# Performance work log

Measured on AMD Instinct MI355X. Metric: run time of the kernel, lower is better.

## Reference

```python
import jax, jax.numpy as jnp
import numpy as np

N_ITEM = 100000
DIV_TRADEOFF = 0.1


def setup_inputs() -> dict:
    key = jax.random.key(0)
    ks = jax.random.split(key, 9)
    B, K, L, D_LLM, H = 512, 8, 50, 768, 128
    return {
        "user_id": jax.random.randint(ks[0], (B,), 0, 50000),
        "base_model_preds": jax.random.randint(ks[1], (B, K, L), 0, N_ITEM + 1),
        "preference_in": jax.random.normal(ks[2], (B, H), jnp.float32),
        "pos_label": jax.random.normal(ks[3], (B, K), jnp.float32),
        "neg_label": jax.random.normal(ks[4], (B, K), jnp.float32),
        "user_embeddings": jax.random.normal(ks[5], (50000, H), jnp.float32) * 0.01,
        "item_embeddings": jax.random.normal(ks[6], (N_ITEM + 1, D_LLM), jnp.float32) * 0.02,
        "W_proj": jax.random.normal(ks[7], (D_LLM, H), jnp.float32) * (1.0 / np.sqrt(D_LLM)),
        "b_proj": jax.random.normal(ks[8], (H,), jnp.float32) * 0.01,
    }


def reference(user_id, base_model_preds, preference_in, pos_label, neg_label,
              user_embeddings, item_embeddings, W_proj, b_proj):
    B, K, L = base_model_preds.shape
    # masked gather-embed: ids outside (0, n_item] map to a zero row
    valid = (base_model_preds > 0) & (base_model_preds <= N_ITEM)
    safe_ids = jnp.where(valid, base_model_preds, 0)
    focus_llm = item_embeddings[safe_ids] * valid[..., None].astype(item_embeddings.dtype)  # [B,K,L,D_llm]
    # linear projection to hidden (bias applied everywhere, matching nn.Linear on zeroed rows)
    bm = jnp.einsum('bkld,dh->bklh', focus_llm, W_proj) + b_proj  # [B,K,L,H]
    # time-decay weighted sum over sequence positions
    time_w = 1.0 / jnp.log2(jnp.arange(L, dtype=jnp.float32) + 2.0)  # [L]
    basemodel_emb = jnp.einsum('bklh,l->bkh', bm, time_w)  # [B,K,H]
    # preference = DIEN(...) + user_emb  (DIEN output modeled by preference_in)
    preference = preference_in + user_embeddings[user_id]  # [B,H]
    wgts_org = jnp.einsum('bkh,bh->bk', basemodel_emb, preference)
    wgts = jax.nn.softmax(wgts_org, axis=-1)  # [B,K]
    pos_scores = jnp.sum(pos_label * wgts, axis=1)
    neg_scores = jnp.sum(neg_label * wgts, axis=1)
    loss = -jnp.sum(jax.nn.log_sigmoid(pos_scores - neg_scores))
    # diversity regularizer (use_div=True)
    cov_wgt = jax.lax.stop_gradient(wgts[:, None, :] + wgts[:, :, None])  # [B,K,K]
    cov_mask = 1.0 - jnp.eye(K, dtype=wgts.dtype)  # [K,K]
    gram = jnp.einsum('bih,bjh->bij', basemodel_emb, basemodel_emb) ** 2
    loss_div = DIV_TRADEOFF * jnp.mean(cov_mask[None] * gram * cov_wgt)
    return loss + loss_div
```

## Files before the change

### kernel.cpp

```cpp
#include <hip/hip_runtime.h>
#include <math.h>

#define B_SZ 512
#define K_SZ 8
#define L_SZ 50
#define DLLM 768
#define H_SZ 128
#define N_ITEM 100000
#define DIV_TRADEOFF 0.1f
#define M_PAD 100032

typedef float  f32x4 __attribute__((ext_vector_type(4)));
typedef short  bf16x8 __attribute__((ext_vector_type(8)));
typedef unsigned int u32x4 __attribute__((ext_vector_type(4)));
typedef unsigned short u16x8 __attribute__((ext_vector_type(8)));

__device__ __forceinline__ unsigned short f2bf(float f) {
    unsigned u = __float_as_uint(f);
    u += 0x7fffu + ((u >> 16) & 1u);
    return (unsigned short)(u >> 16);
}

__device__ __forceinline__ void gload_lds16(const void* g, void* l) {
    __builtin_amdgcn_global_load_lds(
        (const __attribute__((address_space(1))) unsigned*)g,
        (__attribute__((address_space(3))) unsigned*)l, 16, 0, 0);
}

__global__ __launch_bounds__(256) void k_wt(
    const float* __restrict__ W,
    unsigned short* __restrict__ Wt,
    float* __restrict__ out)
{
    __shared__ float tile[64][65];
    const int kb = blockIdx.x >> 1;
    const int nb = blockIdx.x & 1;
    const int t  = threadIdx.x;
    if (blockIdx.x == 0 && t == 0) out[0] = 0.0f;

    const int r  = t >> 2;
    const int c0 = (t & 3) * 16;
    #pragma unroll
    for (int j = 0; j < 4; ++j) {
        const float4 v = *(const float4*)(W + (size_t)(kb * 64 + r) * H_SZ + nb * 64 + c0 + j * 4);
        tile[r][c0 + j * 4 + 0] = v.x;
        tile[r][c0 + j * 4 + 1] = v.y;
        tile[r][c0 + j * 4 + 2] = v.z;
        tile[r][c0 + j * 4 + 3] = v.w;
    }
    __syncthreads();
    const int n  = t >> 2;
    const int k0 = (t & 3) * 16;
    u16x8 lo, hi;
    #pragma unroll
    for (int j = 0; j < 8; ++j) lo[j] = f2bf(tile[k0 + j][n]);
    #pragma unroll
    for (int j = 0; j < 8; ++j) hi[j] = f2bf(tile[k0 + 8 + j][n]);
    unsigned short* dst = Wt + (size_t)(nb * 64 + n) * DLLM + kb * 64 + k0;
    *(u16x8*)(dst)     = lo;
    *(u16x8*)(dst + 8) = hi;
}

__global__ __launch_bounds__(256) void k_proj(
    const float* __restrict__ item,
    const unsigned short* __restrict__ Wt,
    unsigned short* __restrict__ projb)
{
    __shared__ unsigned short As[2][64 * 64];
    __shared__ unsigned short Bs[3][128 * 64];

    const int t    = threadIdx.x;
    const int brow = blockIdx.x * 64;
    const int w    = t >> 6;
    const int lane = t & 63;
    const int nl   = lane & 15;
    const int g    = lane >> 4;
    const int key  = nl & 7;
    const int r    = w * 16 + nl;

    const int b_nsub = (lane >> 3);
    const int b_gl   = lane & 7;
    const int b_key  = b_nsub & 7;
    auto STAGE_B = [&](int d, int c) {
        const int kc = c * 64;
        #pragma unroll
        for (int i = 0; i < 4; ++i) {
            const int n_t = w * 32 + i * 8 + b_nsub;
            const int kb  = (b_gl ^ b_key) * 8;
            gload_lds16(Wt + (size_t)n_t * DLLM + kc + kb,
                        &Bs[d][w * 2048 + i * 512]);
        }
    };

    const int ar    = t >> 2;
    const int aseg  = t & 3;
    const int akey  = ar & 7;
    const int arowS = (brow + ar <= N_ITEM) ? (brow + ar) : N_ITEM;
    const float* __restrict__ asrc = item + (size_t)arowS * DLLM + aseg * 16;

    f32x4 La[4];
    auto A_ISSUE = [&](int c) {
        const float* p = asrc + c * 64;
        #pragma unroll
        for (int j = 0; j < 4; ++j) La[j] = *(const f32x4*)(p + j * 4);
    };
    auto A_WRITE = [&](int d) {
        unsigned p0, p1, p2, p3, p4, p5, p6, p7;
        asm("v_cvt_pk_bf16_f32 %0, %1, %2" : "=v"(p0) : "v"(La[0].x), "v"(La[0].y));
        asm("v_cvt_pk_bf16_f32 %0, %1, %2" : "=v"(p1) : "v"(La[0].z), "v"(La[0].w));
        asm("v_cvt_pk_bf16_f32 %0, %1, %2" : "=v"(p2) : "v"(La[1].x), "v"(La[1].y));
        asm("v_cvt_pk_bf16_f32 %0, %1, %2" : "=v"(p3) : "v"(La[1].z), "v"(La[1].w));
        asm("v_cvt_pk_bf16_f32 %0, %1, %2" : "=v"(p4) : "v"(La[2].x), "v"(La[2].y));
        asm("v_cvt_pk_bf16_f32 %0, %1, %2" : "=v"(p5) : "v"(La[2].z), "v"(La[2].w));
        asm("v_cvt_pk_bf16_f32 %0, %1, %2" : "=v"(p6) : "v"(La[3].x), "v"(La[3].y));
        asm("v_cvt_pk_bf16_f32 %0, %1, %2" : "=v"(p7) : "v"(La[3].z), "v"(La[3].w));
        u32x4 d0; d0[0] = p0; d0[1] = p1; d0[2] = p2; d0[3] = p3;
        u32x4 d1; d1[0] = p4; d1[1] = p5; d1[2] = p6; d1[3] = p7;
        char* base = (char*)&As[d][0] + ar * 128;
        *(u32x4*)(base + (((aseg * 2    ) ^ akey) << 4)) = d0;
        *(u32x4*)(base + (((aseg * 2 + 1) ^ akey) << 4)) = d1;
    };

    f32x4 acc[8];
    #pragma unroll
    for (int i = 0; i < 8; ++i) acc[i] = (f32x4){0.f, 0.f, 0.f, 0.f};

    A_ISSUE(0);
    STAGE_B(0, 0);
    STAGE_B(1, 1);
    asm volatile("s_waitcnt vmcnt(8)" ::: "memory");
    __builtin_amdgcn_sched_barrier(0);
    A_WRITE(0);
    asm volatile("s_waitcnt vmcnt(4) lgkmcnt(0)" ::: "memory");
    __builtin_amdgcn_s_barrier();
    __builtin_amdgcn_sched_barrier(0);

    for (int c = 0; c < 12; ++c) {
        if (c < 11) A_ISSUE(c + 1);
        if (c < 10) STAGE_B((c + 2) % 3, c + 2);
        __builtin_amdgcn_sched_barrier(0);

        const unsigned short* Asc = &As[c & 1][0];
        const unsigned short* Bsc = &Bs[c % 3][0];
        #pragma unroll
        for (int ks = 0; ks < 2; ++ks) {
            const int q = (ks * 4 + g) ^ key;
            const bf16x8 af = *(const bf16x8*)((const char*)Asc + r * 128 + (q << 4));
            #pragma unroll
            for (int nt = 0; nt < 8; ++nt) {
                const bf16x8 b = *(const bf16x8*)&Bsc[(nt * 16 + nl) * 64 + 8 * q];
                acc[nt] = __builtin_amdgcn_mfma_f32_16x16x32_bf16(af, b, acc[nt], 0, 0, 0);
            }
        }

        if (c < 11) {
            if (c < 10) asm volatile("s_waitcnt vmcnt(4)" ::: "memory");
            else        asm volatile("s_waitcnt vmcnt(0)" ::: "memory");
            __builtin_amdgcn_sched_barrier(0);
            A_WRITE((c + 1) & 1);
            asm volatile("s_waitcnt lgkmcnt(0)" ::: "memory");
            __builtin_amdgcn_s_barrier();
            __builtin_amdgcn_sched_barrier(0);
        }
    }

    const int rbase = brow + w * 16 + 4 * g;
    #pragma unroll
    for (int nt = 0; nt < 8; ++nt) {
        #pragma unroll
        for (int rr = 0; rr < 4; ++rr) {
            projb[(size_t)(rbase + rr) * H_SZ + nt * 16 + nl] = f2bf(acc[nt][rr]);
        }
    }
}

__global__ __launch_bounds__(512) void k_gloss(
    const int* __restrict__ preds,
    const unsigned short* __restrict__ projb,
    const float* __restrict__ bproj,
    const int* __restrict__ user_id, const float* __restrict__ pref_in,
    const float* __restrict__ pos_label, const float* __restrict__ neg_label,
    const float* __restrict__ user_emb,
    float* __restrict__ out)
{
    const int b    = blockIdx.x;
    const int tid  = threadIdx.x;
    const int wv   = tid >> 6;
    const int lane = tid & 63;
    const int h2   = lane * 2;

    __shared__ float e[K_SZ][H_SZ + 1];
    __shared__ float pref[H_SZ];
    __shared__ float sdot[K_SZ];
    __shared__ float wg[K_SZ];
    __shared__ float lossb_s;

    {
        const int* __restrict__ p = preds + ((size_t)b * K_SZ + wv) * L_SZ;
        constexpr int PF = 8;
        unsigned buf[PF];
        float wgt[PF];
        #pragma unroll
        for (int i = 0; i < PF; ++i) {
            const int id = p[i];
            const bool v = (id > 0) && (id <= N_ITEM);
            wgt[i] = v ? (1.0f / log2f((float)(i + 2))) : 0.0f;
            buf[i] = *(const unsigned*)(projb + (size_t)(v ? id : 0) * H_SZ + h2);
        }
        float a0 = 0.f, a1 = 0.f;
        #pragma unroll
        for (int l = 0; l < L_SZ; ++l) {
            const int s = l % PF;
            const unsigned u = buf[s];
            const float w = wgt[s];
            if (l + PF < L_SZ) {
                const int id = p[l + PF];
                const bool v = (id > 0) && (id <= N_ITEM);
                wgt[s] = v ? (1.0f / log2f((float)(l + PF + 2))) : 0.0f;
                buf[s] = *(const unsigned*)(projb + (size_t)(v ? id : 0) * H_SZ + h2);
            }
            a0 += w * __uint_as_float(u << 16);
            a1 += w * __uint_as_float(u & 0xffff0000u);
        }
        float sumw = 0.f;
        #pragma unroll
        for (int l = 0; l < L_SZ; ++l) sumw += 1.0f / log2f((float)(l + 2));
        e[wv][h2]     = a0 + bproj[h2]     * sumw;
        e[wv][h2 + 1] = a1 + bproj[h2 + 1] * sumw;
    }
    if (tid < H_SZ) {
        const int uid = user_id[b];
        pref[tid] = pref_in[(size_t)b * H_SZ + tid] + user_emb[(size_t)uid * H_SZ + tid];
    }
    __syncthreads();

    if (tid < 256) {
        const int k = tid >> 5;
        const int l32 = tid & 31;
        float s = e[k][l32] * pref[l32] + e[k][l32 + 32] * pref[l32 + 32]
                + e[k][l32 + 64] * pref[l32 + 64] + e[k][l32 + 96] * pref[l32 + 96];
        #pragma unroll
        for (int m = 16; m >= 1; m >>= 1) s += __shfl_xor(s, m, 64);
        if (l32 == 0) sdot[k] = s;
    }
    __syncthreads();

    if (tid == 0) {
        float mx = sdot[0];
        #pragma unroll
        for (int k = 1; k < K_SZ; ++k) mx = fmaxf(mx, sdot[k]);
        float sum = 0.f; float ex[K_SZ];
        #pragma unroll
        for (int k = 0; k < K_SZ; ++k) { ex[k] = expf(sdot[k] - mx); sum += ex[k]; }
        float ps = 0.f, ns = 0.f;
        #pragma unroll
        for (int k = 0; k < K_SZ; ++k) {
            const float w = ex[k] / sum;
            wg[k] = w;
            ps += pos_label[(size_t)b * K_SZ + k] * w;
            ns += neg_label[(size_t)b * K_SZ + k] * w;
        }
        const float x = ps - ns;
        lossb_s = fmaxf(-x, 0.f) + log1pf(expf(-fabsf(x)));
    }
    __syncthreads();

    if (tid < 64) {
        const int i = tid >> 3;
        const int j = tid & 7;
        float gsum = 0.f;
        for (int h = 0; h < H_SZ; ++h) gsum += e[i][h] * e[j][h];
        float v = (i != j) ? (gsum * gsum * (wg[i] + wg[j])) : 0.f;
        #pragma unroll
        for (int m = 32; m >= 1; m >>= 1) v += __shfl_xor(v, m, 64);
        if (tid == 0) {
            const float mean_div = v / (float)(B_SZ * K_SZ * K_SZ);
            atomicAdd(out, lossb_s + DIV_TRADEOFF * mean_div);
        }
    }
}

__global__ __launch_bounds__(192) void k_gather_fb(
    const int* __restrict__ preds, const float* __restrict__ item,
    float* __restrict__ wf, float* __restrict__ out)
{
    const int bk  = blockIdx.x;
    const int tid = threadIdx.x;
    if (bk == 0 && tid == 0) out[0] = 0.0f;
    const int* __restrict__ p = preds + (size_t)bk * L_SZ;
    const float* __restrict__ ibase = item + (size_t)tid * 4;
    float4 acc = make_float4(0.f, 0.f, 0.f, 0.f);
    constexpr int PF = 8;
    float4 buf[PF]; float wgt[PF];
    #pragma unroll
    for (int i = 0; i < PF; ++i) {
        const int id = p[i];
        const bool v = (id > 0) && (id <= N_ITEM);
        wgt[i] = v ? (1.0f / log2f((float)(i + 2))) : 0.0f;
        buf[i] = *(const float4*)(ibase + (size_t)(v ? id : 0) * DLLM);
    }
    #pragma unroll
    for (int l = 0; l < L_SZ; ++l) {
        const int s = l % PF;
        const float4 v4 = buf[s];
        const float  w  = wgt[s];
        if (l + PF < L_SZ) {
            const int id = p[l + PF];
            const bool v = (id > 0) && (id <= N_ITEM);
            wgt[s] = v ? (1.0f / log2f((float)(l + PF + 2))) : 0.0f;
            buf[s] = *(const float4*)(ibase + (size_t)(v ? id : 0) * DLLM);
        }
        acc.x += w * v4.x; acc.y += w * v4.y; acc.z += w * v4.z; acc.w += w * v4.w;
    }
    *(float4*)(wf + (size_t)bk * DLLM + (size_t)tid * 4) = acc;
}

__global__ __launch_bounds__(256) void k_projloss_fb(
    const float* __restrict__ wf, const float* __restrict__ W,
    const float* __restrict__ bproj, const int* __restrict__ user_id,
    const float* __restrict__ pref_in, const float* __restrict__ pos_label,
    const float* __restrict__ neg_label, const float* __restrict__ user_emb,
    float* __restrict__ out)
{
    const int b   = blockIdx.x;
    const int tid = threadIdx.x;
    const int c   = tid & (H_SZ - 1);
    const int rg  = tid >> 7;
    __shared__ float A[K_SZ][H_SZ];
    __shared__ float e[K_SZ][H_SZ + 1];
    __shared__ float pref[H_SZ];
    __shared__ float sdot[K_SZ];
    __shared__ float wg[K_SZ];
    __shared__ float lossb_s;
    float acc[4] = {0.f, 0.f, 0.f, 0.f};
    const size_t rowbase = (size_t)b * K_SZ;
    for (int kb = 0; kb < DLLM; kb += H_SZ) {
        __syncthreads();
        {
            const int r  = tid >> 5;
            const int kk = (tid & 31) * 4;
            *(float4*)&A[r][kk] = *(const float4*)(wf + (rowbase + r) * DLLM + kb + kk);
        }
        __syncthreads();
        #pragma unroll 4
        for (int k = 0; k < H_SZ; k += 4) {
            const float4 a0 = *(const float4*)&A[rg][k];
            const float4 a1 = *(const float4*)&A[rg + 2][k];
            const float4 a2 = *(const float4*)&A[rg + 4][k];
            const float4 a3 = *(const float4*)&A[rg + 6][k];
            const float* Wp = W + (size_t)(kb + k) * H_SZ + c;
            const float w0 = Wp[0]; const float w1 = Wp[H_SZ];
            const float w2 = Wp[2 * H_SZ]; const float w3 = Wp[3 * H_SZ];
            acc[0] += a0.x * w0 + a0.y * w1 + a0.z * w2 + a0.w * w3;
            acc[1] += a1.x * w0 + a1.y * w1 + a1.z * w2 + a1.w * w3;
            acc[2] += a2.x * w0 + a2.y * w1 + a2.z * w2 + a2.w * w3;
            acc[3] += a3.x * w0 + a3.y * w1 + a3.z * w2 + a3.w * w3;
        }
    }
    float sumw = 0.f;
    #pragma unroll
    for (int l = 0; l < L_SZ; ++l) sumw += 1.0f / log2f((float)(l + 2));
    const float bterm = bproj[c] * sumw;
    #pragma unroll
    for (int ri = 0; ri < 4; ++ri) e[rg + 2 * ri][c] = acc[ri] + bterm;
    if (tid < H_SZ) {
        const int uid = user_id[b];
        pref[tid] = pref_in[(size_t)b * H_SZ + tid] + user_emb[(size_t)uid * H_SZ + tid];
    }
    __syncthreads();
    {
        const int k    = tid >> 5;
        const int lane = tid & 31;
        float s = e[k][lane] * pref[lane] + e[k][lane + 32] * pref[lane + 32]
                + e[k][lane + 64] * pref[lane + 64] + e[k][lane + 96] * pref[lane + 96];
        #pragma unroll
        for (int m = 16; m >= 1; m >>= 1) s += __shfl_xor(s, m, 64);
        if (lane == 0) sdot[k] = s;
    }
    __syncthreads();
    if (tid == 0) {
        float mx = sdot[0];
        #pragma unroll
        for (int k = 1; k < K_SZ; ++k) mx = fmaxf(mx, sdot[k]);
        float sum = 0.f; float ex[K_SZ];
        #pragma unroll
        for (int k = 0; k < K_SZ; ++k) { ex[k] = expf(sdot[k] - mx); sum += ex[k]; }
        float ps = 0.f, ns = 0.f;
        #pragma unroll
        for (int k = 0; k < K_SZ; ++k) {
            const float w = ex[k] / sum;
            wg[k] = w;
            ps += pos_label[(size_t)b * K_SZ + k] * w;
            ns += neg_label[(size_t)b * K_SZ + k] * w;
        }
        const float x = ps - ns;
        lossb_s = fmaxf(-x, 0.f) + log1pf(expf(-fabsf(x)));
    }
    __syncthreads();
    if (tid < 64) {
        const int i = tid >> 3;
        const int j = tid & 7;
        float g = 0.f;
        for (int h = 0; h < H_SZ; ++h) g += e[i][h] * e[j][h];
        float v = (i != j) ? (g * g * (wg[i] + wg[j])) : 0.f;
        #pragma unroll
        for (int m = 32; m >= 1; m >>= 1) v += __shfl_xor(v, m, 64);
        if (tid == 0) {
            const float mean_div = v / (float)(B_SZ * K_SZ * K_SZ);
            atomicAdd(out, lossb_s + DIV_TRADEOFF * mean_div);
        }
    }
}

extern "C" void kernel_launch(void* const* d_in, const int* in_sizes, int n_in,
                              void* d_out, int out_size, void* d_ws, size_t ws_size,
                              hipStream_t stream) {
    const int*   user_id   = (const int*)  d_in[0];
    const int*   preds     = (const int*)  d_in[1];
    const float* pref_in   = (const float*)d_in[2];
    const float* pos_label = (const float*)d_in[3];
    const float* neg_label = (const float*)d_in[4];
    const float* user_emb  = (const float*)d_in[5];
    const float* item_emb  = (const float*)d_in[6];
    const float* W_proj    = (const float*)d_in[7];
    const float* b_proj    = (const float*)d_in[8];

    float* out = (float*)d_out;

    const size_t projb_bytes = (size_t)M_PAD * H_SZ * sizeof(unsigned short);
    const size_t wt_off      = projb_bytes;
    const size_t wt_bytes    = (size_t)H_SZ * DLLM * sizeof(unsigned short);
    const size_t need        = wt_off + wt_bytes;

    if (ws_size >= need) {
        unsigned short* projb = (unsigned short*)d_ws;
        unsigned short* Wt    = (unsigned short*)((char*)d_ws + wt_off);

        k_wt<<<24, 256, 0, stream>>>(W_proj, Wt, out);
        k_proj<<<M_PAD / 64, 256, 0, stream>>>(item_emb, Wt, projb);
        k_gloss<<<B_SZ, 512, 0, stream>>>(preds, projb, b_proj, user_id, pref_in,
                                          pos_label, neg_label, user_emb, out);
    } else {
        float* wf = (float*)d_ws;
        k_gather_fb<<<B_SZ * K_SZ, 192, 0, stream>>>(preds, item_emb, wf, out);
        k_projloss_fb<<<B_SZ, 256, 0, stream>>>(wf, W_proj, b_proj, user_id, pref_in,
                                                pos_label, neg_label, user_emb, out);
    }
}
```

Baseline: 106.7 us.

## Widen projection GEMM K-chunk to 128 and single-buffer W tiles

The item-projection GEMM now walks K in 6 chunks of 128 instead of 12 chunks of 64. A stays double-buffered in registers and LDS, while the triple-buffered B (weight) tiles become a single 128x128 LDS buffer with a 16-way XOR swizzle. Fewer chunks means fewer barriers and waits per block. The catch is that B loads are no longer prefetched ahead: each new B tile is issued only after the previous compute finishes, followed by a full vmcnt(0) wait, which exposes global-load latency.

```diff
diff --git a/kernel.cpp b/kernel.cpp
--- a/kernel.cpp
+++ b/kernel.cpp
@@ -66,8 +66,8 @@
     const unsigned short* __restrict__ Wt,
     unsigned short* __restrict__ projb)
 {
-    __shared__ unsigned short As[2][64 * 64];
-    __shared__ unsigned short Bs[3][128 * 64];
+    __shared__ unsigned short As[2][64 * 128];
+    __shared__ unsigned short Bs[128 * 128];
 
     const int t    = threadIdx.x;
     const int brow = blockIdx.x * 64;
@@ -75,50 +75,45 @@
     const int lane = t & 63;
     const int nl   = lane & 15;
     const int g    = lane >> 4;
-    const int key  = nl & 7;
     const int r    = w * 16 + nl;
 
-    const int b_nsub = (lane >> 3);
-    const int b_gl   = lane & 7;
-    const int b_key  = b_nsub & 7;
-    auto STAGE_B = [&](int d, int c) {
-        const int kc = c * 64;
-        #pragma unroll
-        for (int i = 0; i < 4; ++i) {
-            const int n_t = w * 32 + i * 8 + b_nsub;
-            const int kb  = (b_gl ^ b_key) * 8;
-            gload_lds16(Wt + (size_t)n_t * DLLM + kc + kb,
-                        &Bs[d][w * 2048 + i * 512]);
+    const int b_row16 = lane >> 4;
+    const int b_gran  = lane & 15;
+    auto STAGE_B = [&](int c) {
+        const int kc = c * 128;
+        #pragma unroll
+        for (int i = 0; i < 8; ++i) {
+            const int n_t = w * 32 + i * 4 + b_row16;
+            const int src_g = b_gran ^ (n_t & 15);
+            gload_lds16(Wt + (size_t)n_t * DLLM + kc + src_g * 8,
+                        (char*)Bs + w * 8192 + i * 1024);
         }
     };
 
     const int ar    = t >> 2;
     const int aseg  = t & 3;
-    const int akey  = ar & 7;
+    const int akey  = ar & 15;
     const int arowS = (brow + ar <= N_ITEM) ? (brow + ar) : N_ITEM;
-    const float* __restrict__ asrc = item + (size_t)arowS * DLLM + aseg * 16;
-
-    f32x4 La[4];
+    const float* __restrict__ asrc = item + (size_t)arowS * DLLM + aseg * 32;
+
+    f32x4 La[8];
     auto A_ISSUE = [&](int c) {
-        const float* p = asrc + c * 64;
-        #pragma unroll
-        for (int j = 0; j < 4; ++j) La[j] = *(const f32x4*)(p + j * 4);
+        const float* p = asrc + c * 128;
+        #pragma unroll
+        for (int j = 0; j < 8; ++j) La[j] = *(const f32x4*)(p + j * 4);
     };
     auto A_WRITE = [&](int d) {
-        unsigned p0, p1, p2, p3, p4, p5, p6, p7;
-        asm("v_cvt_pk_bf16_f32 %0, %1, %2" : "=v"(p0) : "v"(La[0].x), "v"(La[0].y));
-        asm("v_cvt_pk_bf16_f32 %0, %1, %2" : "=v"(p1) : "v"(La[0].z), "v"(La[0].w));
-        asm("v_cvt_pk_bf16_f32 %0, %1, %2" : "=v"(p2) : "v"(La[1].x), "v"(La[1].y));
-        asm("v_cvt_pk_bf16_f32 %0, %1, %2" : "=v"(p3) : "v"(La[1].z), "v"(La[1].w));
-        asm("v_cvt_pk_bf16_f32 %0, %1, %2" : "=v"(p4) : "v"(La[2].x), "v"(La[2].y));
-        asm("v_cvt_pk_bf16_f32 %0, %1, %2" : "=v"(p5) : "v"(La[2].z), "v"(La[2].w));
-        asm("v_cvt_pk_bf16_f32 %0, %1, %2" : "=v"(p6) : "v"(La[3].x), "v"(La[3].y));
-        asm("v_cvt_pk_bf16_f32 %0, %1, %2" : "=v"(p7) : "v"(La[3].z), "v"(La[3].w));
-        u32x4 d0; d0[0] = p0; d0[1] = p1; d0[2] = p2; d0[3] = p3;
-        u32x4 d1; d1[0] = p4; d1[1] = p5; d1[2] = p6; d1[3] = p7;
-        char* base = (char*)&As[d][0] + ar * 128;
-        *(u32x4*)(base + (((aseg * 2    ) ^ akey) << 4)) = d0;
-        *(u32x4*)(base + (((aseg * 2 + 1) ^ akey) << 4)) = d1;
+        char* base = (char*)&As[d][0] + ar * 256;
+        #pragma unroll
+        for (int q = 0; q < 4; ++q) {
+            unsigned p0, p1, p2, p3;
+            asm("v_cvt_pk_bf16_f32 %0, %1, %2" : "=v"(p0) : "v"(La[2*q].x),   "v"(La[2*q].y));
+            asm("v_cvt_pk_bf16_f32 %0, %1, %2" : "=v"(p1) : "v"(La[2*q].z),   "v"(La[2*q].w));
+            asm("v_cvt_pk_bf16_f32 %0, %1, %2" : "=v"(p2) : "v"(La[2*q+1].x), "v"(La[2*q+1].y));
+            asm("v_cvt_pk_bf16_f32 %0, %1, %2" : "=v"(p3) : "v"(La[2*q+1].z), "v"(La[2*q+1].w));
+            u32x4 d0; d0[0] = p0; d0[1] = p1; d0[2] = p2; d0[3] = p3;
+            *(u32x4*)(base + (((aseg * 4 + q) ^ akey) << 4)) = d0;
+        }
     };
 
     f32x4 acc[8];
@@ -126,39 +121,40 @@
     for (int i = 0; i < 8; ++i) acc[i] = (f32x4){0.f, 0.f, 0.f, 0.f};
 
     A_ISSUE(0);
-    STAGE_B(0, 0);
-    STAGE_B(1, 1);
+    STAGE_B(0);
     asm volatile("s_waitcnt vmcnt(8)" ::: "memory");
     __builtin_amdgcn_sched_barrier(0);
     A_WRITE(0);
-    asm volatile("s_waitcnt vmcnt(4) lgkmcnt(0)" ::: "memory");
+    asm volatile("s_waitcnt vmcnt(0) lgkmcnt(0)" ::: "memory");
     __builtin_amdgcn_s_barrier();
     __builtin_amdgcn_sched_barrier(0);
 
-    for (int c = 0; c < 12; ++c) {
-        if (c < 11) A_ISSUE(c + 1);
-        if (c < 10) STAGE_B((c + 2) % 3, c + 2);
+    for (int c = 0; c < 6; ++c) {
+        if (c < 5) A_ISSUE(c + 1);
         __builtin_amdgcn_sched_barrier(0);
 
         const unsigned short* Asc = &As[c & 1][0];
-        const unsigned short* Bsc = &Bs[c % 3][0];
-        #pragma unroll
-        for (int ks = 0; ks < 2; ++ks) {
-            const int q = (ks * 4 + g) ^ key;
-            const bf16x8 af = *(const bf16x8*)((const char*)Asc + r * 128 + (q << 4));
+        #pragma unroll
+        for (int ks = 0; ks < 4; ++ks) {
+            const int q = (ks * 4 + g) ^ nl;
+            const bf16x8 af = *(const bf16x8*)((const char*)Asc + r * 256 + (q << 4));
             #pragma unroll
             for (int nt = 0; nt < 8; ++nt) {
-                const bf16x8 b = *(const bf16x8*)&Bsc[(nt * 16 + nl) * 64 + 8 * q];
+                const bf16x8 b = *(const bf16x8*)((const char*)Bs
+                                    + (nt * 16 + nl) * 256 + (q << 4));
                 acc[nt] = __builtin_amdgcn_mfma_f32_16x16x32_bf16(af, b, acc[nt], 0, 0, 0);
             }
         }
 
-        if (c < 11) {
-            if (c < 10) asm volatile("s_waitcnt vmcnt(4)" ::: "memory");
-            else        asm volatile("s_waitcnt vmcnt(0)" ::: "memory");
+        if (c < 5) {
+            asm volatile("s_waitcnt lgkmcnt(0)" ::: "memory");
+            __builtin_amdgcn_s_barrier();
+            __builtin_amdgcn_sched_barrier(0);
+            STAGE_B(c + 1);
+            asm volatile("s_waitcnt vmcnt(8)" ::: "memory");
             __builtin_amdgcn_sched_barrier(0);
             A_WRITE((c + 1) & 1);
-            asm volatile("s_waitcnt lgkmcnt(0)" ::: "memory");
+            asm volatile("s_waitcnt vmcnt(0) lgkmcnt(0)" ::: "memory");
             __builtin_amdgcn_s_barrier();
             __builtin_amdgcn_sched_barrier(0);
         }
```

After: 110.4 us. 1.03x slower.
